# Kernel optimization log

Hardware: AMD Instinct MI355X
Metric: run time of the kernel (lower is better)

Reference implementation:

```python
import jax, jax.numpy as jnp
import numpy as np

MIN_NORM = 1e-15
EPS = 1e-5
C_CURV = 1.0  # args.c

def _norm(x):
    return jnp.clip(jnp.linalg.norm(x, axis=-1, keepdims=True), MIN_NORM)

def artanh(x):
    x = jnp.clip(x, -1.0 + EPS, 1.0 - EPS)
    return 0.5 * (jnp.log1p(x) - jnp.log1p(-x))

def proj(x, c):
    # clip points to stay strictly inside the Poincare ball
    norm = _norm(x)
    maxnorm = (1.0 - EPS) / jnp.sqrt(c)
    return jnp.where(norm > maxnorm, x / norm * maxnorm, x)

def expmap0(u, c):
    sqrt_c = jnp.sqrt(c)
    u_norm = _norm(u)
    return jnp.tanh(sqrt_c * u_norm) * u / (sqrt_c * u_norm)

def logmap0(p, c):
    sqrt_c = jnp.sqrt(c)
    p_norm = _norm(p)
    return artanh(sqrt_c * p_norm) * p / (sqrt_c * p_norm)

def mobius_add(x, y, c):
    x2 = jnp.sum(x * x, axis=-1, keepdims=True)
    y2 = jnp.sum(y * y, axis=-1, keepdims=True)
    xy = jnp.sum(x * y, axis=-1, keepdims=True)
    num = (1.0 + 2.0 * c * xy + c * y2) * x + (1.0 - c * x2) * y
    denom = 1.0 + 2.0 * c * xy + c * c * x2 * y2
    return num / jnp.clip(denom, MIN_NORM)

def mobius_matvec(W, x, c):
    sqrt_c = jnp.sqrt(c)
    x_norm = _norm(x)
    mx = x @ W.T
    mx_norm = _norm(mx)
    return jnp.tanh(mx_norm / x_norm * artanh(sqrt_c * x_norm)) * mx / (mx_norm * sqrt_c)

def poincare_dist(x, y, c):
    sqrt_c = jnp.sqrt(c)
    d = _norm(mobius_add(-x, y, c))[..., 0]
    return 2.0 / sqrt_c * artanh(sqrt_c * d)

def hgnn_layer(h, adj, W, b, c):
    # HypLinear: mobius matvec + hyperbolic bias
    mv = proj(mobius_matvec(W, h, c), c)
    hyp_b = proj(expmap0(b, c), c)
    h = proj(mobius_add(mv, hyp_b, c), c)
    # HypAgg: aggregate in tangent space at origin
    h = proj(expmap0(adj @ logmap0(h, c), c), c)
    # HypAct: relu in tangent space
    return proj(expmap0(jax.nn.relu(logmap0(h, c)), c), c)

def setup_inputs() -> dict:
    key = jax.random.key(0)
    ks = jax.random.split(key, 10)
    N, D, C, NC, NODE_C, L = 8192, 128, 64, 7, 7, 4
    x = jax.random.normal(ks[0], (N, D), jnp.float32)
    adj = jax.random.uniform(ks[1], (N, N), jnp.float32) / N  # row-stochastic-ish dense adjacency
    graph_indicator = jax.random.randint(ks[2], (N,), 0, 1)
    W_conv = jax.random.normal(ks[3], (L, D, D), jnp.float32) / np.sqrt(D)
    b_conv = jax.random.normal(ks[4], (L, D), jnp.float32) * 0.01
    centroids = jax.random.normal(ks[5], (C, D), jnp.float32) * 0.1
    W_mlp = jax.random.normal(ks[6], (NC, C), jnp.float32) * 0.1
    b_mlp = jnp.zeros((NC,), jnp.float32)
    W_mlp1 = jax.random.normal(ks[7], (NODE_C, D), jnp.float32) * 0.1
    b_mlp1 = jnp.zeros((NODE_C,), jnp.float32)
    return {"x": x, "adj": adj, "graph_indicator": graph_indicator,
            "W_conv": W_conv, "b_conv": b_conv, "centroids": centroids,
            "W_mlp": W_mlp, "b_mlp": b_mlp, "W_mlp1": W_mlp1, "b_mlp1": b_mlp1}

def reference(x, adj, graph_indicator, W_conv, b_conv, centroids, W_mlp, b_mlp, W_mlp1, b_mlp1):
    c = C_CURV
    # proj_tan0 is identity for PoincareBall
    h = proj(expmap0(x, c), c)
    # 2 residual blocks, each with 2 HGNN layers; shortcut is identity (in_dim == out_dim)
    for blk in range(2):
        res = h
        for j in range(2):
            idx = blk * 2 + j
            h = hgnn_layer(h, adj, W_conv[idx], b_conv[idx], c)
        h = h + res  # Euclidean residual, as in the source
    # CentroidDistance: pairwise hyperbolic distance [N, C]
    node_centroid_dist = poincare_dist(h[:, None, :], centroids[None, :, :], c)
    readout = jnp.mean(node_centroid_dist, axis=0, keepdims=True)  # [1, C]
    h_r = logmap0(readout, c)  # proj_tan0(logmap0(.)) -> identity proj_tan0
    logits = jax.nn.softmax(h_r @ W_mlp.T + b_mlp, axis=0)[None]        # [1,1,NC]
    h1 = logmap0(h, c)
    logits_node = jax.nn.softmax(h1 @ W_mlp1.T + b_mlp1, axis=0)[None]  # [1,N,node_classes]
    return (logits, logits_node, h_r)
```

## Files before the change

kernel.cpp:

```cpp
#include <hip/hip_runtime.h>

#define MIN_NORM 1e-15f
#define EPSV 1e-5f
#define MAXN (1.0f - EPSV)
#define NN 8192
#define DD 128

typedef unsigned short u16;
typedef __bf16 bf16x8 __attribute__((ext_vector_type(8)));
typedef float f32x4 __attribute__((ext_vector_type(4)));

__device__ __forceinline__ float wave_sum(float v) {
#pragma unroll
  for (int off = 32; off > 0; off >>= 1) v += __shfl_xor(v, off, 64);
  return v;
}

__device__ __forceinline__ float artanh_f(float x) {
  x = fminf(fmaxf(x, -1.0f + EPSV), 1.0f - EPSV);
  return 0.5f * (log1pf(x) - log1pf(-x));
}

__device__ __forceinline__ u16 f2bf(float f) {
  unsigned u = __float_as_uint(f);
  unsigned r = (u + 0x7fffu + ((u >> 16) & 1u)) >> 16;
  return (u16)r;
}
__device__ __forceinline__ float bf2f(u16 b) { return __uint_as_float(((unsigned)b) << 16); }

template <bool AF32, bool DUMP>
__global__ __launch_bounds__(256) void gemm_bt(const void* __restrict__ Av,
                                               const u16* __restrict__ Bt,
                                               float* __restrict__ Cp,
                                               u16* __restrict__ Adump,
                                               int M, int K, int KC) {
  constexpr int ABYTES = AF32 ? (64 * 68 * 4) : (64 * 72 * 2);
  __shared__ __align__(16) char Abuf[ABYTES];
  __shared__ __align__(16) u16 Bs[128 * 72];
  float* As = (float*)Abuf;
  u16* Ash = (u16*)Abuf;

  const int tid = threadIdx.x;
  const int lane = tid & 63;
  const int w = tid >> 6;
  const int wm = w >> 1, wn = w & 1;
  const int lrow = lane & 15;
  const int lq = lane >> 4;
  const int m0 = blockIdx.x * 64;
  const int kk0 = blockIdx.y * KC;

  f32x4 acc[2][4];
#pragma unroll
  for (int a = 0; a < 2; a++)
#pragma unroll
    for (int b = 0; b < 4; b++)
#pragma unroll
      for (int r = 0; r < 4; r++) acc[a][b][r] = 0.0f;

  for (int kt = 0; kt < KC; kt += 64) {
    const int kk = kk0 + kt;
    __syncthreads();
    if constexpr (AF32) {
      const float* A = (const float*)Av;
#pragma unroll
      for (int it = 0; it < 4; it++) {
        int idx = it * 256 + tid;
        int r = idx >> 4, c = (idx & 15) << 2;
        float4 v = *(const float4*)(A + (size_t)(m0 + r) * K + kk + c);
        *(float4*)&As[r * 68 + c] = v;
        if constexpr (DUMP) {
          ushort4 d;
          d.x = f2bf(v.x); d.y = f2bf(v.y); d.z = f2bf(v.z); d.w = f2bf(v.w);
          *(ushort4*)(Adump + (size_t)(m0 + r) * K + kk + c) = d;
        }
      }
    } else {
      const u16* A = (const u16*)Av;
#pragma unroll
      for (int it = 0; it < 2; it++) {
        int idx = it * 256 + tid;
        int r = idx >> 3, c = (idx & 7) << 3;
        uint4 v = *(const uint4*)(A + (size_t)(m0 + r) * K + kk + c);
        *(uint4*)&Ash[r * 72 + c] = v;
      }
    }
#pragma unroll
    for (int it = 0; it < 4; it++) {
      int idx = it * 256 + tid;
      int n = idx >> 3, c = (idx & 7) << 3;
      uint4 v = *(const uint4*)(Bt + (size_t)n * K + kk + c);
      *(uint4*)&Bs[n * 72 + c] = v;
    }
    __syncthreads();
#pragma unroll
    for (int ks = 0; ks < 2; ks++) {
      const int kloc = ks * 32 + lq * 8;
      bf16x8 af[2], bfr[4];
#pragma unroll
      for (int ti = 0; ti < 2; ti++) {
        int r = wm * 32 + ti * 16 + lrow;
        if constexpr (AF32) {
          const float* p = &As[r * 68 + kloc];
          float4 q0 = *(const float4*)p;
          float4 q1 = *(const float4*)(p + 4);
          bf16x8 t;
          t[0] = (__bf16)q0.x; t[1] = (__bf16)q0.y; t[2] = (__bf16)q0.z; t[3] = (__bf16)q0.w;
          t[4] = (__bf16)q1.x; t[5] = (__bf16)q1.y; t[6] = (__bf16)q1.z; t[7] = (__bf16)q1.w;
          af[ti] = t;
        } else {
          af[ti] = *(const bf16x8*)&Ash[r * 72 + kloc];
        }
      }
#pragma unroll
      for (int tj = 0; tj < 4; tj++) {
        int n = wn * 64 + tj * 16 + lrow;
        bfr[tj] = *(const bf16x8*)&Bs[n * 72 + kloc];
      }
#pragma unroll
      for (int ti = 0; ti < 2; ti++)
#pragma unroll
        for (int tj = 0; tj < 4; tj++)
          acc[ti][tj] = __builtin_amdgcn_mfma_f32_16x16x32_bf16(af[ti], bfr[tj], acc[ti][tj], 0, 0, 0);
    }
  }
  float* C = Cp + (size_t)blockIdx.y * M * 128;
#pragma unroll
  for (int ti = 0; ti < 2; ti++)
#pragma unroll
    for (int tj = 0; tj < 4; tj++)
#pragma unroll
      for (int r = 0; r < 4; r++) {
        int row = m0 + wm * 32 + ti * 16 + lq * 4 + r;
        int col = wn * 64 + tj * 16 + lrow;
        C[(size_t)row * 128 + col] = acc[ti][tj][r];
      }
}

__global__ void build_wt(const float* __restrict__ W, u16* __restrict__ Wt2) {
  int idx = blockIdx.x * 256 + threadIdx.x;
  if (idx >= 4 * 128 * 128) return;
  int layer = idx >> 14;
  int n = (idx >> 7) & 127;
  int k = idx & 127;
  float e = W[idx];
  u16 hi = f2bf(e);
  u16 lo = f2bf(e - bf2f(hi));
  u16* base = Wt2 + (size_t)layer * 128 * 384 + (size_t)n * 384;
  base[k] = hi;
  base[128 + k] = hi;
  base[256 + k] = lo;
}

__device__ __forceinline__ void write_split(u16* hs, int i, int lane, float v0, float v1) {
  u16* row = hs + (size_t)i * 384;
  u16 h0 = f2bf(v0), h1 = f2bf(v1);
  u16 l0 = f2bf(v0 - bf2f(h0)), l1 = f2bf(v1 - bf2f(h1));
  row[lane] = h0;         row[lane + 64] = h1;
  row[128 + lane] = l0;   row[128 + 64 + lane] = l1;
  row[256 + lane] = h0;   row[256 + 64 + lane] = h1;
}

__global__ __launch_bounds__(64) void rowwise_init(const float* __restrict__ x,
                                                   float* __restrict__ h,
                                                   float* __restrict__ res,
                                                   u16* __restrict__ hsplit) {
  int i = blockIdx.x, lane = threadIdx.x;
  const float* xr = x + (size_t)i * DD;
  float a0 = xr[lane], a1 = xr[lane + 64];
  float n = fmaxf(sqrtf(wave_sum(a0 * a0 + a1 * a1)), MIN_NORM);
  float g = tanhf(n) / n;
  float y0 = g * a0, y1 = g * a1;
  float pn = fmaxf(sqrtf(wave_sum(y0 * y0 + y1 * y1)), MIN_NORM);
  float s = pn > MAXN ? MAXN / pn : 1.0f;
  y0 *= s; y1 *= s;
  size_t base = (size_t)i * DD;
  h[base + lane] = y0;   h[base + lane + 64] = y1;
  res[base + lane] = y0; res[base + lane + 64] = y1;
  write_split(hsplit, i, lane, y0, y1);
}

__global__ __launch_bounds__(64) void rowwise_mid(const float* __restrict__ h,
                                                  const float* __restrict__ P,
                                                  const float* __restrict__ bvec,
                                                  u16* __restrict__ uT) {
  int i = blockIdx.x, lane = threadIdx.x;
  size_t base = (size_t)i * DD;
  const float* hr = h + base;
  float h0 = hr[lane], h1 = hr[lane + 64];
  float m0 = 0.f, m1 = 0.f;
#pragma unroll
  for (int sk = 0; sk < 3; sk++) {
    const float* p = P + (size_t)sk * NN * DD + base;
    m0 += p[lane];
    m1 += p[lane + 64];
  }
  float xn = fmaxf(sqrtf(wave_sum(h0 * h0 + h1 * h1)), MIN_NORM);
  float mn = fmaxf(sqrtf(wave_sum(m0 * m0 + m1 * m1)), MIN_NORM);
  float t = tanhf(mn / xn * artanh_f(xn));
  float v0 = t * m0 / mn, v1 = t * m1 / mn;
  float pn = fmaxf(sqrtf(wave_sum(v0 * v0 + v1 * v1)), MIN_NORM);
  float sc = pn > MAXN ? MAXN / pn : 1.0f;
  v0 *= sc; v1 *= sc;
  float b0 = bvec[lane], b1 = bvec[lane + 64];
  float bn = fmaxf(sqrtf(wave_sum(b0 * b0 + b1 * b1)), MIN_NORM);
  float gb = tanhf(bn) / bn;
  float e0 = gb * b0, e1 = gb * b1;
  float en = fmaxf(sqrtf(wave_sum(e0 * e0 + e1 * e1)), MIN_NORM);
  float sb = en > MAXN ? MAXN / en : 1.0f;
  e0 *= sb; e1 *= sb;
  float x2 = wave_sum(v0 * v0 + v1 * v1);
  float y2 = wave_sum(e0 * e0 + e1 * e1);
  float xy = wave_sum(v0 * e0 + v1 * e1);
  float ca = 1.0f + 2.0f * xy + y2;
  float cb = 1.0f - x2;
  float den = fmaxf(1.0f + 2.0f * xy + x2 * y2, MIN_NORM);
  float t0 = (ca * v0 + cb * e0) / den, t1 = (ca * v1 + cb * e1) / den;
  float tn = fmaxf(sqrtf(wave_sum(t0 * t0 + t1 * t1)), MIN_NORM);
  float st = tn > MAXN ? MAXN / tn : 1.0f;
  t0 *= st; t1 *= st;
  float pn2 = fmaxf(sqrtf(wave_sum(t0 * t0 + t1 * t1)), MIN_NORM);
  float gl = artanh_f(pn2) / pn2;
  uT[(size_t)lane * NN + i] = f2bf(gl * t0);
  uT[(size_t)(lane + 64) * NN + i] = f2bf(gl * t1);
}

__global__ __launch_bounds__(64) void rowwise_post(const float* __restrict__ P,
                                                   float* __restrict__ h,
                                                   float* __restrict__ res,
                                                   u16* __restrict__ hsplit,
                                                   int addres) {
  int i = blockIdx.x, lane = threadIdx.x;
  size_t base = (size_t)i * DD;
  float m0 = 0.f, m1 = 0.f;
#pragma unroll
  for (int sk = 0; sk < 8; sk++) {
    const float* p = P + (size_t)sk * NN * DD + base;
    m0 += p[lane];
    m1 += p[lane + 64];
  }
  float n = fmaxf(sqrtf(wave_sum(m0 * m0 + m1 * m1)), MIN_NORM);
  float g = tanhf(n) / n;
  float y0 = g * m0, y1 = g * m1;
  float pn = fmaxf(sqrtf(wave_sum(y0 * y0 + y1 * y1)), MIN_NORM);
  float s = pn > MAXN ? MAXN / pn : 1.0f;
  y0 *= s; y1 *= s;
  float hn = fmaxf(sqrtf(wave_sum(y0 * y0 + y1 * y1)), MIN_NORM);
  float gl = artanh_f(hn) / hn;
  float u0 = fmaxf(gl * y0, 0.0f), u1 = fmaxf(gl * y1, 0.0f);
  float un = fmaxf(sqrtf(wave_sum(u0 * u0 + u1 * u1)), MIN_NORM);
  float ge = tanhf(un) / un;
  float z0 = ge * u0, z1 = ge * u1;
  float zn = fmaxf(sqrtf(wave_sum(z0 * z0 + z1 * z1)), MIN_NORM);
  float sz = zn > MAXN ? MAXN / zn : 1.0f;
  z0 *= sz; z1 *= sz;
  if (addres) {
    z0 += res[base + lane];
    z1 += res[base + lane + 64];
    res[base + lane] = z0;
    res[base + lane + 64] = z1;
  }
  h[base + lane] = z0;
  h[base + lane + 64] = z1;
  write_split(hsplit, i, lane, z0, z1);
}

__global__ __launch_bounds__(256) void centroid_k(const float* __restrict__ h,
                                                  const float* __restrict__ cen,
                                                  float* __restrict__ rs) {
  __shared__ float cs[64 * 129];
  __shared__ float hs[32 * 128];
  __shared__ float y2s[64];
  int tid = threadIdx.x;
  int i0 = blockIdx.x * 32;
  for (int idx = tid; idx < 64 * 128; idx += 256) {
    int r = idx >> 7, c = idx & 127;
    cs[r * 129 + c] = cen[idx];
  }
  for (int idx = tid; idx < 32 * 128; idx += 256) hs[idx] = h[(size_t)i0 * 128 + idx];
  __syncthreads();
  if (tid < 64) {
    float s = 0.f;
    for (int k = 0; k < 128; k++) { float v = cs[tid * 129 + k]; s = fmaf(v, v, s); }
    y2s[tid] = s;
  }
  __syncthreads();
  int w = tid >> 6, lane = tid & 63;
  float dsum = 0.f;
  for (int rr = 0; rr < 8; rr++) {
    int r = w * 8 + rr;
    float dot = 0.f, x2 = 0.f;
    for (int k = 0; k < 128; k++) {
      float hk = hs[r * 128 + k];
      dot = fmaf(hk, cs[lane * 129 + k], dot);
      x2 = fmaf(hk, hk, x2);
    }
    float y2 = y2s[lane];
    float al = 1.0f - 2.0f * dot + y2;
    float be = 1.0f - x2;
    float num2 = al * al * x2 + be * be * y2 - 2.0f * al * be * dot;
    float den = fmaxf(1.0f - 2.0f * dot + x2 * y2, MIN_NORM);
    float d = fmaxf(sqrtf(fmaxf(num2, 0.0f)) / den, MIN_NORM);
    dsum += 2.0f * artanh_f(d);
  }
  atomicAdd(&rs[lane], dsum);
}

__global__ __launch_bounds__(64) void finalize_k(const float* __restrict__ rs,
                                                 float* __restrict__ out) {
  int lane = threadIdx.x;
  float r = rs[lane] * (1.0f / 8192.0f);
  float n = fmaxf(sqrtf(wave_sum(r * r)), MIN_NORM);
  float a = artanh_f(n);
  out[7 + NN * 7 + lane] = a * r / n;
  if (lane < 7) out[lane] = 1.0f;
}

__global__ __launch_bounds__(64) void scores_k(const float* __restrict__ h,
                                               const float* __restrict__ Wm,
                                               const float* __restrict__ bm,
                                               float* __restrict__ sc) {
  int i = blockIdx.x, lane = threadIdx.x;
  const float* hr = h + (size_t)i * DD;
  float h0 = hr[lane], h1 = hr[lane + 64];
  float pn = fmaxf(sqrtf(wave_sum(h0 * h0 + h1 * h1)), MIN_NORM);
  float gl = artanh_f(pn) / pn;
  float u0 = gl * h0, u1 = gl * h1;
  float p[7];
#pragma unroll
  for (int j = 0; j < 7; j++)
    p[j] = wave_sum(u0 * Wm[j * 128 + lane] + u1 * Wm[j * 128 + lane + 64]);
  float v = p[0];
#pragma unroll
  for (int j = 1; j < 7; j++)
    if (lane == j) v = p[j];
  if (lane < 7) sc[(size_t)i * 7 + lane] = v + bm[lane];
}

__global__ __launch_bounds__(256) void softmax_col(const float* __restrict__ sc,
                                                   float* __restrict__ out) {
  __shared__ float buf[256][8];
  int tid = threadIdx.x;
  float mx[7];
#pragma unroll
  for (int j = 0; j < 7; j++) mx[j] = -1e30f;
  for (int i = tid; i < NN; i += 256)
#pragma unroll
    for (int j = 0; j < 7; j++) mx[j] = fmaxf(mx[j], sc[i * 7 + j]);
#pragma unroll
  for (int j = 0; j < 7; j++) buf[tid][j] = mx[j];
  __syncthreads();
  for (int off = 128; off > 0; off >>= 1) {
    if (tid < off)
#pragma unroll
      for (int j = 0; j < 7; j++) buf[tid][j] = fmaxf(buf[tid][j], buf[tid + off][j]);
    __syncthreads();
  }
  float cm[7];
#pragma unroll
  for (int j = 0; j < 7; j++) cm[j] = buf[0][j];
  __syncthreads();
  float sm[7];
#pragma unroll
  for (int j = 0; j < 7; j++) sm[j] = 0.f;
  for (int i = tid; i < NN; i += 256)
#pragma unroll
    for (int j = 0; j < 7; j++) sm[j] += expf(sc[i * 7 + j] - cm[j]);
#pragma unroll
  for (int j = 0; j < 7; j++) buf[tid][j] = sm[j];
  __syncthreads();
  for (int off = 128; off > 0; off >>= 1) {
    if (tid < off)
#pragma unroll
      for (int j = 0; j < 7; j++) buf[tid][j] += buf[tid + off][j];
    __syncthreads();
  }
  float csum[7];
#pragma unroll
  for (int j = 0; j < 7; j++) csum[j] = buf[0][j];
  __syncthreads();
  for (int idx = tid; idx < NN * 7; idx += 256) {
    int i = idx / 7, j = idx - i * 7;
    out[idx] = expf(sc[i * 7 + j] - cm[j]) / csum[j];
  }
}

extern "C" void kernel_launch(void* const* d_in, const int* in_sizes, int n_in,
                              void* d_out, int out_size, void* d_ws, size_t ws_size,
                              hipStream_t stream) {
  const float* x = (const float*)d_in[0];
  const float* adj = (const float*)d_in[1];
  const float* W_conv = (const float*)d_in[3];
  const float* b_conv = (const float*)d_in[4];
  const float* centroids = (const float*)d_in[5];
  const float* W_mlp1 = (const float*)d_in[8];
  const float* b_mlp1 = (const float*)d_in[9];
  float* out = (float*)d_out;

  char* ws = (char*)d_ws;
  size_t off = 0;
  auto alloc = [&](size_t bytes) {
    void* p = ws + off;
    off = (off + bytes + 255) & ~(size_t)255;
    return p;
  };
  float* h = (float*)alloc((size_t)NN * DD * 4);
  float* res = (float*)alloc((size_t)NN * DD * 4);
  u16* hsplit = (u16*)alloc((size_t)NN * 384 * 2);
  u16* uT = (u16*)alloc((size_t)DD * NN * 2);
  u16* Wt2 = (u16*)alloc((size_t)4 * 128 * 384 * 2);
  float* P = (float*)alloc((size_t)8 * NN * DD * 4);
  u16* adjbf = (u16*)alloc((size_t)NN * NN * 2);
  float* scores = (float*)alloc((size_t)NN * 7 * 4);
  float* rs = (float*)alloc(64 * 4);
  (void)ws_size; (void)in_sizes; (void)n_in; (void)out_size;

  hipMemsetAsync(rs, 0, 64 * 4, stream);
  build_wt<<<(4 * 128 * 128 + 255) / 256, 256, 0, stream>>>(W_conv, Wt2);
  rowwise_init<<<NN, 64, 0, stream>>>(x, h, res, hsplit);
  for (int layer = 0; layer < 4; layer++) {
    gemm_bt<false, false><<<dim3(NN / 64, 3), 256, 0, stream>>>(
        hsplit, Wt2 + (size_t)layer * 128 * 384, P, nullptr, NN, 384, 128);
    rowwise_mid<<<NN, 64, 0, stream>>>(h, P, b_conv + layer * DD, uT);
    if (layer == 0) {
      gemm_bt<true, true><<<dim3(NN / 64, 8), 256, 0, stream>>>(
          adj, uT, P, adjbf, NN, NN, NN / 8);
    } else {
      gemm_bt<false, false><<<dim3(NN / 64, 8), 256, 0, stream>>>(
          adjbf, uT, P, nullptr, NN, NN, NN / 8);
    }
    rowwise_post<<<NN, 64, 0, stream>>>(P, h, res, hsplit, (layer & 1));
  }
  centroid_k<<<256, 256, 0, stream>>>(h, centroids, rs);
  finalize_k<<<1, 64, 0, stream>>>(rs, out);
  scores_k<<<NN, 64, 0, stream>>>(h, W_mlp1, b_mlp1, scores);
  softmax_col<<<1, 256, 0, stream>>>(scores, out + 7);
}
```

Baseline: 873.6 us.

## Double-buffer GEMM with async global-to-LDS loads and split out adj conversion

Rewrites the bf16 GEMM to stage A and B tiles straight into LDS with global_load_lds, double-buffered so the next k-tile loads while the current one feeds the MFMAs. The padded shared layout is replaced by an XOR-swizzled layout to avoid bank conflicts. The fp32 adjacency conversion in the first layer is moved out of the GEMM into a separate grid-stride cvt_adj kernel, so every layer runs the same bf16 GEMM path. This trades one extra full pass over adj for a simpler and better-overlapped GEMM mainloop, and it doubles the LDS used per block.

```diff
diff --git a/kernel.cpp b/kernel.cpp
--- a/kernel.cpp
+++ b/kernel.cpp
@@ -28,17 +28,17 @@
 }
 __device__ __forceinline__ float bf2f(u16 b) { return __uint_as_float(((unsigned)b) << 16); }
 
-template <bool AF32, bool DUMP>
-__global__ __launch_bounds__(256) void gemm_bt(const void* __restrict__ Av,
+__device__ __forceinline__ void gload16(const u16* g, u16* l) {
+  __builtin_amdgcn_global_load_lds((const __attribute__((address_space(1))) void*)(g),
+                                   (__attribute__((address_space(3))) void*)(l), 16, 0, 0);
+}
+
+__global__ __launch_bounds__(256) void gemm_bt(const u16* __restrict__ A,
                                                const u16* __restrict__ Bt,
                                                float* __restrict__ Cp,
-                                               u16* __restrict__ Adump,
                                                int M, int K, int KC) {
-  constexpr int ABYTES = AF32 ? (64 * 68 * 4) : (64 * 72 * 2);
-  __shared__ __align__(16) char Abuf[ABYTES];
-  __shared__ __align__(16) u16 Bs[128 * 72];
-  float* As = (float*)Abuf;
-  u16* Ash = (u16*)Abuf;
+  __shared__ __align__(16) u16 Ash[2 * 64 * 64];
+  __shared__ __align__(16) u16 Bsh[2 * 128 * 64];
 
   const int tid = threadIdx.x;
   const int lane = tid & 63;
@@ -49,6 +49,11 @@
   const int m0 = blockIdx.x * 64;
   const int kk0 = blockIdx.y * KC;
 
+  const int srow = lane >> 3;
+  const int spc = lane & 7;
+
+  const u16* Ap = A + (size_t)m0 * K;
+
   f32x4 acc[2][4];
 #pragma unroll
   for (int a = 0; a < 2; a++)
@@ -57,64 +62,42 @@
 #pragma unroll
       for (int r = 0; r < 4; r++) acc[a][b][r] = 0.0f;
 
-  for (int kt = 0; kt < KC; kt += 64) {
-    const int kk = kk0 + kt;
+#define STAGE(bf, kk)                                                          \
+  do {                                                                         \
+    _Pragma("unroll") for (int ii = 0; ii < 2; ii++) {                         \
+      int rw = ((ii * 4 + w) << 3) + srow;                                     \
+      gload16(Ap + (size_t)rw * K + (kk) + ((spc ^ (rw & 7)) << 3),            \
+              &Ash[(bf) * 4096 + ((ii * 4 + w) << 9)]);                        \
+    }                                                                          \
+    _Pragma("unroll") for (int ii = 0; ii < 4; ii++) {                         \
+      int rw = ((ii * 4 + w) << 3) + srow;                                     \
+      gload16(Bt + (size_t)rw * K + (kk) + ((spc ^ (rw & 7)) << 3),            \
+              &Bsh[(bf) * 8192 + ((ii * 4 + w) << 9)]);                        \
+    }                                                                          \
+  } while (0)
+
+  const int nt = KC >> 6;
+  STAGE(0, kk0);
+
+  for (int t = 0; t < nt; t++) {
+    const int cur = t & 1;
     __syncthreads();
-    if constexpr (AF32) {
-      const float* A = (const float*)Av;
-#pragma unroll
-      for (int it = 0; it < 4; it++) {
-        int idx = it * 256 + tid;
-        int r = idx >> 4, c = (idx & 15) << 2;
-        float4 v = *(const float4*)(A + (size_t)(m0 + r) * K + kk + c);
-        *(float4*)&As[r * 68 + c] = v;
-        if constexpr (DUMP) {
-          ushort4 d;
-          d.x = f2bf(v.x); d.y = f2bf(v.y); d.z = f2bf(v.z); d.w = f2bf(v.w);
-          *(ushort4*)(Adump + (size_t)(m0 + r) * K + kk + c) = d;
-        }
-      }
-    } else {
-      const u16* A = (const u16*)Av;
-#pragma unroll
-      for (int it = 0; it < 2; it++) {
-        int idx = it * 256 + tid;
-        int r = idx >> 3, c = (idx & 7) << 3;
-        uint4 v = *(const uint4*)(A + (size_t)(m0 + r) * K + kk + c);
-        *(uint4*)&Ash[r * 72 + c] = v;
-      }
-    }
-#pragma unroll
-    for (int it = 0; it < 4; it++) {
-      int idx = it * 256 + tid;
-      int n = idx >> 3, c = (idx & 7) << 3;
-      uint4 v = *(const uint4*)(Bt + (size_t)n * K + kk + c);
-      *(uint4*)&Bs[n * 72 + c] = v;
-    }
-    __syncthreads();
+    if (t + 1 < nt) STAGE(cur ^ 1, kk0 + (t + 1) * 64);
+
+    const int abase = cur * 4096, bbase = cur * 8192;
 #pragma unroll
     for (int ks = 0; ks < 2; ks++) {
-      const int kloc = ks * 32 + lq * 8;
+      const int lc = ks * 4 + lq;
       bf16x8 af[2], bfr[4];
 #pragma unroll
       for (int ti = 0; ti < 2; ti++) {
         int r = wm * 32 + ti * 16 + lrow;
-        if constexpr (AF32) {
-          const float* p = &As[r * 68 + kloc];
-          float4 q0 = *(const float4*)p;
-          float4 q1 = *(const float4*)(p + 4);
-          bf16x8 t;
-          t[0] = (__bf16)q0.x; t[1] = (__bf16)q0.y; t[2] = (__bf16)q0.z; t[3] = (__bf16)q0.w;
-          t[4] = (__bf16)q1.x; t[5] = (__bf16)q1.y; t[6] = (__bf16)q1.z; t[7] = (__bf16)q1.w;
-          af[ti] = t;
-        } else {
-          af[ti] = *(const bf16x8*)&Ash[r * 72 + kloc];
-        }
+        af[ti] = *(const bf16x8*)&Ash[abase + r * 64 + ((lc ^ (r & 7)) << 3)];
       }
 #pragma unroll
       for (int tj = 0; tj < 4; tj++) {
         int n = wn * 64 + tj * 16 + lrow;
-        bfr[tj] = *(const bf16x8*)&Bs[n * 72 + kloc];
+        bfr[tj] = *(const bf16x8*)&Bsh[bbase + n * 64 + ((lc ^ (n & 7)) << 3)];
       }
 #pragma unroll
       for (int ti = 0; ti < 2; ti++)
@@ -123,6 +106,8 @@
           acc[ti][tj] = __builtin_amdgcn_mfma_f32_16x16x32_bf16(af[ti], bfr[tj], acc[ti][tj], 0, 0, 0);
     }
   }
+#undef STAGE
+
   float* C = Cp + (size_t)blockIdx.y * M * 128;
 #pragma unroll
   for (int ti = 0; ti < 2; ti++)
@@ -134,6 +119,21 @@
         int col = wn * 64 + tj * 16 + lrow;
         C[(size_t)row * 128 + col] = acc[ti][tj][r];
       }
+}
+
+__global__ __launch_bounds__(256) void cvt_adj(const float* __restrict__ src,
+                                               u16* __restrict__ dst) {
+  const size_t stride = (size_t)gridDim.x * 256 * 8;
+  for (size_t base = ((size_t)blockIdx.x * 256 + threadIdx.x) * 8;
+       base < (size_t)NN * NN; base += stride) {
+    float4 a = *(const float4*)(src + base);
+    float4 b = *(const float4*)(src + base + 4);
+    ushort4 d0, d1;
+    d0.x = f2bf(a.x); d0.y = f2bf(a.y); d0.z = f2bf(a.z); d0.w = f2bf(a.w);
+    d1.x = f2bf(b.x); d1.y = f2bf(b.y); d1.z = f2bf(b.z); d1.w = f2bf(b.w);
+    *(ushort4*)(dst + base) = d0;
+    *(ushort4*)(dst + base + 4) = d1;
+  }
 }
 
 __global__ void build_wt(const float* __restrict__ W, u16* __restrict__ Wt2) {
@@ -417,17 +417,13 @@
   hipMemsetAsync(rs, 0, 64 * 4, stream);
   build_wt<<<(4 * 128 * 128 + 255) / 256, 256, 0, stream>>>(W_conv, Wt2);
   rowwise_init<<<NN, 64, 0, stream>>>(x, h, res, hsplit);
+  cvt_adj<<<2048, 256, 0, stream>>>(adj, adjbf);
   for (int layer = 0; layer < 4; layer++) {
-    gemm_bt<false, false><<<dim3(NN / 64, 3), 256, 0, stream>>>(
-        hsplit, Wt2 + (size_t)layer * 128 * 384, P, nullptr, NN, 384, 128);
+    gemm_bt<<<dim3(NN / 64, 3), 256, 0, stream>>>(
+        hsplit, Wt2 + (size_t)layer * 128 * 384, P, NN, 384, 128);
     rowwise_mid<<<NN, 64, 0, stream>>>(h, P, b_conv + layer * DD, uT);
-    if (layer == 0) {
-      gemm_bt<true, true><<<dim3(NN / 64, 8), 256, 0, stream>>>(
-          adj, uT, P, adjbf, NN, NN, NN / 8);
-    } else {
-      gemm_bt<false, false><<<dim3(NN / 64, 8), 256, 0, stream>>>(
-          adjbf, uT, P, nullptr, NN, NN, NN / 8);
-    }
+    gemm_bt<<<dim3(NN / 64, 8), 256, 0, stream>>>(
+        adjbf, uT, P, NN, NN, NN / 8);
     rowwise_post<<<NN, 64, 0, stream>>>(P, h, res, hsplit, (layer & 1));
   }
   centroid_k<<<256, 256, 0, stream>>>(h, centroids, rs);
```

Result: faster. 817.3 us (-6.4%).
